# Performance work log

Measured on AMD Instinct MI355X. Metric: run time of the kernel, lower is better.

Reference implementation:

```python
import jax, jax.numpy as jnp
import numpy as np

B, H, W = 8, 512, 512
N_INST = 8
N_SIGMA = 2
FG_W = 1.0
W_INST, W_VAR, W_SEED = 1.0, 10.0, 1.0


def make_yxm():
    xm = jnp.broadcast_to(jnp.linspace(0.0, 1.0, W)[None, None, :], (1, H, W))
    ym = jnp.broadcast_to(jnp.linspace(0.0, 1.0, H)[None, :, None], (1, H, W))
    return jnp.concatenate([ym, xm], 0)  # [2,H,W]


def lovasz_hinge(logits, labels):
    # logits, labels: [P]; labels in {0,1}
    signs = 2.0 * labels - 1.0
    errors = 1.0 - logits * signs
    order = jnp.argsort(-errors)
    errors_s = errors[order]
    gt_s = labels[order]
    gts = gt_s.sum()
    intersection = gts - jnp.cumsum(gt_s)
    union = gts + jnp.cumsum(1.0 - gt_s)
    jac = 1.0 - intersection / union
    jac = jnp.concatenate([jac[:1], jac[1:] - jac[:-1]])
    return jnp.dot(jax.nn.relu(errors_s), jax.lax.stop_gradient(jac))


def seg_item(pred, inst, label, center_img, yxm):
    spatial_emb = jnp.tanh(pred[0:2]) + yxm            # [2,H,W]
    sigma = jax.nn.sigmoid(pred[2:2 + N_SIGMA])        # [2,H,W]
    seed = jax.nn.sigmoid(pred[2 + N_SIGMA])           # [H,W]
    seed_loss = jnp.sum(jnp.where(label == 0, seed * seed, 0.0))

    def per_inst(iid):
        in_mask = (inst == iid)
        cmask = in_mask & center_img
        valid = (cmask.sum() == 1)                      # exactly one center pixel
        m = in_mask.astype(pred.dtype)
        npix = jnp.maximum(m.sum(), 1.0)
        center = jnp.sum(yxm * cmask, axis=(1, 2))      # [2]
        s_mean = jnp.sum(sigma * m, axis=(1, 2)) / npix # [2]
        var_l = jnp.sum(((sigma - jax.lax.stop_gradient(s_mean)[:, None, None]) ** 2) * m) / (N_SIGMA * npix)
        s = jnp.exp(s_mean * 10.0)
        dist = jnp.exp(-jnp.sum(((spatial_emb - center[:, None, None]) ** 2) * s[:, None, None], axis=0))
        inst_l = lovasz_hinge((dist * 2.0 - 1.0).ravel(), m.ravel())
        seed_l = jnp.sum(((seed - jax.lax.stop_gradient(dist)) ** 2) * m)
        v = valid.astype(pred.dtype)
        return inst_l * v, var_l * v, seed_l * v

    il, vl, sl = jax.vmap(per_inst)(jnp.arange(1, N_INST + 1))
    # NOTE: source never increments obj_count in the seg loop, so no division.
    seed_total = (seed_loss + FG_W * sl.sum()) / (H * W)
    return W_INST * il.sum() + W_VAR * vl.sum() + W_SEED * seed_total


def tra_item(pred, inst, center_img, offset, yxm):
    emb = yxm - jnp.tanh(pred[0:2])
    sigma = jax.nn.sigmoid(pred[2:2 + N_SIGMA])

    def per_inst(iid):
        in_mask = (inst == iid)
        cmask = in_mask & center_img
        center = jnp.sum(yxm * cmask, axis=(1, 2))          # [2]
        off_c = jnp.sum(offset * cmask, axis=(1, 2))        # [2]
        gt_c = center - off_c / 256.0
        valid = (cmask.sum() == 1) & (gt_c.min() >= 0.0) & (gt_c.max() <= 1.0)
        m = in_mask.astype(pred.dtype)
        npix = jnp.maximum(m.sum(), 1.0)
        s_mean = jnp.sum(sigma * m, axis=(1, 2)) / npix
        var_l = jnp.sum(((sigma - jax.lax.stop_gradient(s_mean)[:, None, None]) ** 2) * m)  # sum (not mean)
        s = jnp.exp(s_mean * 10.0)
        dist = jnp.exp(-jnp.sum(((emb - gt_c[:, None, None]) ** 2) * s[:, None, None], axis=0))
        tl = lovasz_hinge((dist * 2.0 - 1.0).ravel(), m.ravel())
        v = valid.astype(pred.dtype)
        return tl * v, var_l * v, v

    tl, vl, vs = jax.vmap(per_inst)(jnp.arange(1, N_INST + 1))
    cnt = jnp.maximum(vs.sum(), 1.0)
    return W_INST * (tl.sum() / cnt) + W_VAR * (vl.sum() / cnt)


def setup_inputs() -> dict:
    key = jax.random.key(0)
    k1, k2, k3 = jax.random.split(key, 3)
    inst = np.zeros((H, W), np.int32)
    cen = np.zeros((H, W), bool)
    for i in range(N_INST):
        ty, tx = i // 2, i % 2
        cy, cx = ty * 128 + 64, tx * 256 + 128
        inst[cy - 40:cy + 40, cx - 40:cx + 40] = i + 1
        cen[cy, cx] = True
    instances = jnp.tile(jnp.asarray(inst)[None], (B, 1, 1))
    center_images = jnp.tile(jnp.asarray(cen)[None], (B, 1, 1))
    labels = (instances > 0).astype(jnp.int32)
    return {
        "segmentation_predictions": jax.random.normal(k1, (B, 3 + N_SIGMA, H, W), jnp.float32),
        "tracking_predictions": jax.random.normal(k2, (B // 2, 2 + N_SIGMA, H, W), jnp.float32),
        "instances": instances,
        "labels": labels,
        "center_images": center_images,
        "offsets": jax.random.normal(k3, (B // 2, 2, H, W), jnp.float32),
    }


def reference(segmentation_predictions, tracking_predictions, instances, labels, center_images, offsets):
    yxm = make_yxm()
    seg = jax.vmap(seg_item, in_axes=(0, 0, 0, 0, None))(
        segmentation_predictions, instances, labels, center_images, yxm)
    half = B // 2
    tra = jax.vmap(tra_item, in_axes=(0, 0, 0, 0, None))(
        tracking_predictions, instances[:half], center_images[:half], offsets, yxm)
    return seg.sum() + tra.sum()
```

## Files before the change

### kernel.cpp

```cpp
#include <hip/hip_runtime.h>
#include <cstdint>
#include <cstddef>

#define HW (512 * 512)
#define NB 128
#define NPAIR 96
#define THRQ 4.9f
#define BSCALE 64.0f
#define RB 128

#define W_HNEG 0
#define W_HPOS (NPAIR * NB)
#define W_SEEDL (NPAIR * NB * 2)
#define W_CNT (W_SEEDL + NPAIR)
#define NZERO (W_CNT + 1)
#define W_PART 24704
#define W_CSUM (W_PART + 12 * 81 * RB)
#define W_PRM (W_CSUM + 12 * 81)
#define W_POUT (W_PRM + 12 * 32)

__device__ __forceinline__ float sigmoidf_(float x) {
    return 1.0f / (1.0f + __expf(-x));
}
__device__ __forceinline__ float tanhf_(float x) {
    float e = __expf(2.0f * x);
    return 1.0f - 2.0f / (e + 1.0f);
}
__device__ __forceinline__ float wred(float v) {
#pragma unroll
    for (int o = 32; o > 0; o >>= 1) v += __shfl_down(v, o, 64);
    return v;
}

__global__ __launch_bounds__(256) void reduce_k(
    const float* __restrict__ segp, const float* __restrict__ trap,
    const int* __restrict__ inst, const int* __restrict__ cen,
    const float* __restrict__ off, float* __restrict__ ws)
{
    __shared__ float wavepart[4][41];
    __shared__ float centacc[40];
    int item = blockIdx.y;
    bool isseg = item < 8;
    int ii = isseg ? item : item - 8;
    int bx = blockIdx.x, tid = threadIdx.x;

    {
        int gb = (item * RB + bx) * 17 + tid;
        if (tid < 17 && gb < NZERO) ws[gb] = 0.0f;
    }
    if (tid < 40) centacc[tid] = 0.0f;
    __syncthreads();

    const float* pb = isseg ? segp + (size_t)item * 5 * HW
                            : trap + (size_t)ii * 4 * HW;
    const int* ib = inst + (size_t)ii * HW;
    const int* cb = cen + (size_t)ii * HW;
    const float* ob = off + (size_t)ii * 2 * HW;

    float npx[8], a0[8], q0[8], a1[8], q1[8];
#pragma unroll
    for (int j = 0; j < 8; j++) { npx[j]=0.f; a0[j]=0.f; q0[j]=0.f; a1[j]=0.f; q1[j]=0.f; }
    float sacc = 0.f;

    int base = bx * 2048;
#pragma unroll
    for (int it = 0; it < 2; ++it) {
        int idx = base + (it * 256 + tid) * 4;
        int4 v4 = *(const int4*)&ib[idx];
        const int vs[4] = { v4.x, v4.y, v4.z, v4.w };
        if (isseg) {
            float4 x4 = *(const float4*)&pb[4 * HW + idx];
            const float ss[4] = { x4.x, x4.y, x4.z, x4.w };
#pragma unroll
            for (int c = 0; c < 4; c++) {
                if (vs[c] == 0) { float sd = sigmoidf_(ss[c]); sacc += sd * sd; }
            }
        }
        if ((v4.x | v4.y | v4.z | v4.w) != 0) {
            int4 c4 = *(const int4*)&cb[idx];
            float4 x2 = *(const float4*)&pb[2 * HW + idx];
            float4 x3 = *(const float4*)&pb[3 * HW + idx];
            const int cs[4] = { c4.x, c4.y, c4.z, c4.w };
            const float s2s[4] = { x2.x, x2.y, x2.z, x2.w };
            const float s3s[4] = { x3.x, x3.y, x3.z, x3.w };
#pragma unroll
            for (int c = 0; c < 4; c++) {
                int v = vs[c];
                if (v == 0) continue;
                float s0 = sigmoidf_(s2s[c]);
                float s1 = sigmoidf_(s3s[c]);
                float s00 = s0 * s0, s11 = s1 * s1;
#pragma unroll
                for (int j = 0; j < 8; j++) {
                    float f = (v == j + 1) ? 1.0f : 0.0f;
                    npx[j] += f;
                    a0[j] += f * s0; q0[j] += f * s00;
                    a1[j] += f * s1; q1[j] += f * s11;
                }
                if (cs[c] != 0 && v >= 1 && v <= 8) {
                    int idxc = idx + c;
                    int cb5 = (v - 1) * 5;
                    int y = idxc >> 9, x = idxc & 511;
                    atomicAdd(&centacc[cb5 + 0], (float)y * (1.0f / 511.0f));
                    atomicAdd(&centacc[cb5 + 1], (float)x * (1.0f / 511.0f));
                    atomicAdd(&centacc[cb5 + 2], 1.0f);
                    if (!isseg) {
                        atomicAdd(&centacc[cb5 + 3], ob[idxc]);
                        atomicAdd(&centacc[cb5 + 4], ob[HW + idxc]);
                    }
                }
            }
        }
    }
    int lane = tid & 63, wave = tid >> 6;
#pragma unroll
    for (int j = 0; j < 8; j++) {
        float r0 = wred(npx[j]), r1 = wred(a0[j]), r2 = wred(q0[j]);
        float r3 = wred(a1[j]), r4 = wred(q1[j]);
        if (lane == 0) {
            wavepart[wave][j * 5 + 0] = r0; wavepart[wave][j * 5 + 1] = r1;
            wavepart[wave][j * 5 + 2] = r2; wavepart[wave][j * 5 + 3] = r3;
            wavepart[wave][j * 5 + 4] = r4;
        }
    }
    {
        float rs = wred(sacc);
        if (lane == 0) wavepart[wave][40] = rs;
    }
    __syncthreads();
    float* pit = ws + W_PART + (size_t)item * 81 * RB;
    if (tid < 40) {
        pit[tid * RB + bx] = wavepart[0][tid] + wavepart[1][tid] + wavepart[2][tid] + wavepart[3][tid];
    } else if (tid == 40) {
        pit[80 * RB + bx] = wavepart[0][40] + wavepart[1][40] + wavepart[2][40] + wavepart[3][40];
    } else if (tid < 81) {
        pit[(tid - 1) * RB + bx] = centacc[tid - 41];
    }
}

__global__ __launch_bounds__(256) void csum_k(float* __restrict__ ws)
{
    __shared__ float csh[81];
    int item = blockIdx.x, tid = threadIdx.x;
    bool isseg = item < 8;
    if (tid < 162) {
        int comp = tid >> 1;
        const float* p = ws + W_PART + (size_t)item * 81 * RB + comp * RB + (tid & 1) * 64;
        float s = 0.f;
#pragma unroll 8
        for (int i = 0; i < 64; i++) s += p[i];
        s += __shfl_xor(s, 1, 64);
        if ((tid & 1) == 0) csh[comp] = s;
    }
    __syncthreads();
    if (tid < 81) ws[W_CSUM + item * 81 + tid] = csh[tid];
    if (tid < 8) {
        int j = tid;
        float np = fmaxf(csh[j * 5], 1.0f);
        float cy = csh[40 + j * 5], cx = csh[40 + j * 5 + 1];
        if (!isseg) {
            cy -= csh[40 + j * 5 + 3] * (1.0f / 256.0f);
            cx -= csh[40 + j * 5 + 4] * (1.0f / 256.0f);
        }
        float* o = ws + W_PRM + item * 32 + j * 4;
        o[0] = cy;
        o[1] = cx;
        o[2] = __expf(10.0f * csh[j * 5 + 1] / np);
        o[3] = __expf(10.0f * csh[j * 5 + 3] / np);
    }
}

__global__ __launch_bounds__(256) void hist_k(
    const float* __restrict__ segp, const float* __restrict__ trap,
    const int* __restrict__ inst, float* __restrict__ ws)
{
    __shared__ unsigned hh[8 * NB + 8];
    __shared__ float4 prmv[8];
    __shared__ unsigned char lut[48 * 64];
    int item = blockIdx.y;
    bool isseg = item < 8;
    int ii = isseg ? item : item - 8;
    int bx = blockIdx.x, tid = threadIdx.x;
    int pairBase = (isseg ? 0 : 64) + ii * 8;

    unsigned* wsu = (unsigned*)ws;
    unsigned* hneg = wsu + W_HNEG;
    unsigned* hpos = wsu + W_HPOS;
    float* seedl = ws + W_SEEDL;

    if (tid < 8) prmv[tid] = ((const float4*)(ws + W_PRM + item * 32))[tid];
    for (int i = tid; i < 8 * NB + 8; i += 256) hh[i] = 0u;
    __syncthreads();
    for (int ci = tid; ci < 48 * 64; ci += 256) {
        int iy = ci >> 6, ix = ci & 63;
        float ey = -1.0f + ((float)iy + 0.5f) * (1.0f / 16.0f);
        float ex = -1.0f + ((float)ix + 0.5f) * (1.0f / 16.0f);
        unsigned mk = 0u;
#pragma unroll
        for (int j = 0; j < 8; j++) {
            float4 P = prmv[j];
            float dy = fmaxf(fabsf(ey - P.x) - (1.0f / 32.0f), 0.0f);
            float dx = fmaxf(fabsf(ex - P.y) - (1.0f / 32.0f), 0.0f);
            if (fmaf(dy * dy, P.z, dx * dx * P.w) <= THRQ) mk |= 1u << j;
        }
        lut[ci] = (unsigned char)mk;
    }
    __syncthreads();

    const float* pb = isseg ? segp + (size_t)item * 5 * HW
                            : trap + (size_t)ii * 4 * HW;
    const int* ib = inst + (size_t)ii * HW;

    int base = bx * 2048;
#pragma unroll
    for (int it = 0; it < 2; ++it) {
        int idx = base + (it * 256 + tid) * 4;
        int4 v4 = *(const int4*)&ib[idx];
        float4 f0 = *(const float4*)&pb[idx];
        float4 f1 = *(const float4*)&pb[HW + idx];
        const int vv[4] = { v4.x, v4.y, v4.z, v4.w };
        const float p0s[4] = { f0.x, f0.y, f0.z, f0.w };
        const float p1s[4] = { f1.x, f1.y, f1.z, f1.w };
#pragma unroll
        for (int c = 0; c < 4; c++) {
            int idxc = idx + c;
            int v = vv[c];
            int y = idxc >> 9, x = idxc & 511;
            float ym = (float)y * (1.0f / 511.0f);
            float xm = (float)x * (1.0f / 511.0f);
            float t0 = tanhf_(p0s[c]), t1 = tanhf_(p1s[c]);
            float e0 = isseg ? (t0 + ym) : (ym - t0);
            float e1 = isseg ? (t1 + xm) : (xm - t1);
            int iy = (int)((e0 + 1.0f) * 16.0f);
            int ix = (int)((e1 + 1.0f) * 16.0f);
            unsigned mask = lut[iy * 64 + ix];
            unsigned vb = (unsigned)(v - 1);
            if (vb < 8u) mask |= 1u << vb;
            while (mask) {
                int j = __ffs(mask) - 1;
                mask &= mask - 1u;
                float4 P = prmv[j];
                float d0 = e0 - P.x, d1 = e1 - P.y;
                float q = fmaf(d0 * d0, P.z, d1 * d1 * P.w);
                bool m = (v == j + 1);
                if (m || (q <= THRQ)) {
                    float dd = __expf(-q);
                    float e = m ? fmaf(-2.0f, dd, 2.0f) : 2.0f * dd;
                    int bin = (int)(e * BSCALE);
                    if (bin > NB - 1) bin = NB - 1;
                    atomicAdd(&hh[j * NB + bin], m ? 0x10000u : 1u);
                    if (m && isseg) {
                        float sd = sigmoidf_(pb[4 * HW + idxc]);
                        float df = sd - dd;
                        atomicAdd((float*)&hh[8 * NB + j], df * df);
                    }
                }
            }
        }
    }
    __syncthreads();
    {
        int g = tid >> 5, gl = tid & 31;
        unsigned s = 0u;
#pragma unroll
        for (int b = 0; b < 4; b++) {
            unsigned hv = hh[g * NB + gl * 4 + b];
            s += (hv & 0xFFFFu) + (hv >> 16);
        }
#pragma unroll
        for (int o = 16; o > 0; o >>= 1) s += __shfl_down(s, o, 32);
        if (gl == 0) atomicAdd(&hh[g * NB], 2048u - s);
    }
    __syncthreads();
    for (int i = tid; i < 8 * NB; i += 256) {
        unsigned hv = hh[i];
        if (hv) {
            int j = i >> 7, b = i & (NB - 1);
            size_t gb = (size_t)(pairBase + j) * NB + b;
            unsigned n = hv & 0xFFFFu, p = hv >> 16;
            if (n) atomicAdd(&hneg[gb], n);
            if (p) atomicAdd(&hpos[gb], p);
        }
    }
    if (isseg && tid < 8) {
        float sv = __uint_as_float(hh[8 * NB + tid]);
        if (sv != 0.0f) atomicAdd(&seedl[pairBase + tid], sv);
    }
}

__global__ __launch_bounds__(64) void scanfin_k(
    float* __restrict__ ws, float* __restrict__ out)
{
    __shared__ float fin[NPAIR * 4 + 8];
    int p = blockIdx.x;
    int lane = threadIdx.x;
    unsigned* wsu = (unsigned*)ws;
    const unsigned* hneg = wsu + W_HNEG;
    const unsigned* hpos = wsu + W_HPOS;
    unsigned* cntr = wsu + W_CNT;

    int item12 = (p < 64) ? (p >> 3) : (8 + ((p - 64) >> 3));
    int j = p & 7;
    const float* cs = ws + W_CSUM + item12 * 81;
    float val = 0.f;
    if (lane < 10) {
        int comp = (lane < 5) ? (j * 5 + lane) : (40 + j * 5 + (lane - 5));
        val = cs[comp];
    }
    float r0 = __shfl(val, 0, 64), r1 = __shfl(val, 1, 64), r2 = __shfl(val, 2, 64);
    float r3 = __shfl(val, 3, 64), r4 = __shfl(val, 4, 64);
    float c0 = __shfl(val, 5, 64), c1 = __shfl(val, 6, 64), c2 = __shfl(val, 7, 64);
    float c3 = __shfl(val, 8, 64), c4 = __shfl(val, 9, 64);

    const unsigned* hn = hneg + (size_t)p * NB;
    const unsigned* hp = hpos + (size_t)p * NB;
    unsigned hnv[2], hpv[2];
    float ck = 0.f, cp = 0.f;
#pragma unroll
    for (int i = 0; i < 2; i++) {
        int bn = NB - 1 - (lane * 2 + i);
        unsigned a = hn[bn], b = hp[bn];
        hnv[i] = a; hpv[i] = b;
        ck += (float)(a + b); cp += (float)b;
    }
    float ik = ck, ip = cp;
#pragma unroll
    for (int o = 1; o < 64; o <<= 1) {
        float nk = __shfl_up(ik, o, 64), np2 = __shfl_up(ip, o, 64);
        if (lane >= o) { ik += nk; ip += np2; }
    }
    float P = __shfl(ip, 63, 64);
    float k = ik - ck, pp = ip - cp;
    float acc = 0.f;
#pragma unroll
    for (int i = 0; i < 2; i++) {
        float cn = (float)hnv[i], cpp = (float)hpv[i];
        float c = cn + cpp;
        if (c > 0.f) {
            float Jb = (k > 0.f) ? (1.0f - (P - pp) / (P + k - pp)) : 0.0f;
            k += c; pp += cpp;
            float Ja = 1.0f - (P - pp) / (P + k - pp);
            int bn = NB - 1 - (lane * 2 + i);
            acc += ((float)bn + 0.5f) * (2.0f / NB) * (Ja - Jb);
        }
    }
    acc = wred(acc);

    if (lane == 0) {
        float np = fmaxf(r0, 1.0f);
        float v0 = fmaxf(r2 - r1 * r1 / np, 0.0f);
        float v1 = fmaxf(r4 - r3 * r3 / np, 0.0f);
        float valid, varl;
        if (p < 64) {
            varl = (v0 + v1) / (2.0f * np);
            valid = (c2 > 0.5f && c2 < 1.5f) ? 1.0f : 0.0f;
        } else {
            varl = v0 + v1;
            float gy = c0 - c3 * (1.0f / 256.0f);
            float gx = c1 - c4 * (1.0f / 256.0f);
            valid = (c2 > 0.5f && c2 < 1.5f &&
                     gy >= 0.0f && gy <= 1.0f && gx >= 0.0f && gx <= 1.0f) ? 1.0f : 0.0f;
        }
        float* po = ws + W_POUT + p * 4;
        po[0] = acc; po[1] = valid; po[2] = varl; po[3] = 0.0f;
    }
    __threadfence();
    unsigned old = 0;
    if (lane == 0) old = atomicAdd(cntr, 1u);
    old = (unsigned)__shfl((int)old, 0, 64);
    if (old != NPAIR - 1) return;
    __threadfence();

    volatile const float* pv = ws + W_POUT;
    volatile const float* sdv = ws + W_SEEDL;
    volatile const float* csv = ws + W_CSUM;
    for (int q = lane; q < NPAIR; q += 64) {
        fin[q * 4 + 0] = pv[q * 4 + 0];
        fin[q * 4 + 1] = pv[q * 4 + 1];
        fin[q * 4 + 2] = pv[q * 4 + 2];
        fin[q * 4 + 3] = sdv[q];
    }
    if (lane < 8) fin[NPAIR * 4 + lane] = csv[lane * 81 + 80];
    __syncthreads();
    if (lane == 0) {
        double total = 0.0;
        for (int b = 0; b < 8; b++) {
            double s = 0.0, sl = 0.0;
            for (int jj = 0; jj < 8; jj++) {
                int pr = b * 8 + jj;
                double v = fin[pr * 4 + 1];
                s += v * ((double)fin[pr * 4 + 0] + 10.0 * (double)fin[pr * 4 + 2]);
                sl += v * (double)fin[pr * 4 + 3];
            }
            total += s + ((double)fin[NPAIR * 4 + b] + sl) / (double)HW;
        }
        for (int tt = 0; tt < 4; tt++) {
            double tl = 0.0, vl = 0.0, cnt = 0.0;
            for (int jj = 0; jj < 8; jj++) {
                int pr = 64 + tt * 8 + jj;
                double v = fin[pr * 4 + 1];
                tl += v * (double)fin[pr * 4 + 0];
                vl += v * (double)fin[pr * 4 + 2];
                cnt += v;
            }
            if (cnt < 1.0) cnt = 1.0;
            total += tl / cnt + 10.0 * vl / cnt;
        }
        *out = (float)total;
    }
}

extern "C" void kernel_launch(void* const* d_in, const int* in_sizes, int n_in,
                              void* d_out, int out_size, void* d_ws, size_t ws_size,
                              hipStream_t stream)
{
    const float* segp = (const float*)d_in[0];
    const float* trap = (const float*)d_in[1];
    const int* inst   = (const int*)d_in[2];
    const int* cen    = (const int*)d_in[4];
    const float* off  = (const float*)d_in[5];
    float* out = (float*)d_out;
    float* ws = (float*)d_ws;

    reduce_k<<<dim3(RB, 12), 256, 0, stream>>>(segp, trap, inst, cen, off, ws);
    csum_k<<<12, 256, 0, stream>>>(ws);
    hist_k<<<dim3(RB, 12), 256, 0, stream>>>(segp, trap, inst, ws);
    scanfin_k<<<NPAIR, 64, 0, stream>>>(ws, out);
}
```

Before: 64.83 us.

## Precompute packed quantized embeddings in first pass and split center accumulation kernel

The first pass now computes the tanh-based spatial embedding and writes it, quantized, together with the instance id into one packed 32-bit word per pixel in the workspace. The histogram pass then reads this single word instead of re-reading two prediction channels and the instance map and recomputing tanh. Center-pixel accumulation moves out of the reduction into a separate cen_k kernel over 8 images, and a zero_k kernel clears the accumulators. This trades extra launches, an extra full-size workspace write and quantization error in the embeddings for fewer reads and less math in the histogram pass.

```diff
diff --git a/kernel.cpp b/kernel.cpp
--- a/kernel.cpp
+++ b/kernel.cpp
@@ -13,11 +13,13 @@
 #define W_HPOS (NPAIR * NB)
 #define W_SEEDL (NPAIR * NB * 2)
 #define W_CNT (W_SEEDL + NPAIR)
-#define NZERO (W_CNT + 1)
-#define W_PART 24704
-#define W_CSUM (W_PART + 12 * 81 * RB)
-#define W_PRM (W_CSUM + 12 * 81)
+#define W_CPAR 24676
+#define W_ZEND (W_CPAR + 320)
+#define W_PART 25088
+#define W_CSUM (W_PART + 12 * 41 * RB)
+#define W_PRM 88560
 #define W_POUT (W_PRM + 12 * 32)
+#define W_EPACK 89344
 
 __device__ __forceinline__ float sigmoidf_(float x) {
     return 1.0f / (1.0f + __expf(-x));
@@ -32,30 +34,58 @@
     return v;
 }
 
-__global__ __launch_bounds__(256) void reduce_k(
+__global__ __launch_bounds__(256) void zero_k(float* __restrict__ ws) {
+    int n = W_ZEND - W_SEEDL;
+    for (int i = threadIdx.x; i < n; i += 256) ws[W_SEEDL + i] = 0.0f;
+}
+
+__global__ __launch_bounds__(256) void cen_k(
+    const int* __restrict__ cen, const int* __restrict__ inst,
+    const float* __restrict__ off, float* __restrict__ ws)
+{
+    int img = blockIdx.y;
+    int idx = (blockIdx.x * 256 + threadIdx.x) * 4;
+    int4 c4 = *(const int4*)&cen[(size_t)img * HW + idx];
+    if ((c4.x | c4.y | c4.z | c4.w) == 0) return;
+    const int cs[4] = { c4.x, c4.y, c4.z, c4.w };
+#pragma unroll
+    for (int c = 0; c < 4; c++) {
+        if (cs[c] == 0) continue;
+        int idxc = idx + c;
+        unsigned v = (unsigned)inst[(size_t)img * HW + idxc];
+        if (v - 1u < 8u) {
+            float* cp = ws + W_CPAR + img * 40 + (v - 1) * 5;
+            int y = idxc >> 9, x = idxc & 511;
+            atomicAdd(cp + 0, (float)y * (1.0f / 511.0f));
+            atomicAdd(cp + 1, (float)x * (1.0f / 511.0f));
+            atomicAdd(cp + 2, 1.0f);
+            if (img < 4) {
+                atomicAdd(cp + 3, off[(size_t)img * 2 * HW + idxc]);
+                atomicAdd(cp + 4, off[(size_t)(img * 2 + 1) * HW + idxc]);
+            }
+        }
+    }
+}
+
+__global__ __launch_bounds__(256) void prep_k(
     const float* __restrict__ segp, const float* __restrict__ trap,
-    const int* __restrict__ inst, const int* __restrict__ cen,
-    const float* __restrict__ off, float* __restrict__ ws)
+    const int* __restrict__ inst, float* __restrict__ ws)
 {
     __shared__ float wavepart[4][41];
-    __shared__ float centacc[40];
     int item = blockIdx.y;
     bool isseg = item < 8;
     int ii = isseg ? item : item - 8;
     int bx = blockIdx.x, tid = threadIdx.x;
 
     {
-        int gb = (item * RB + bx) * 17 + tid;
-        if (tid < 17 && gb < NZERO) ws[gb] = 0.0f;
-    }
-    if (tid < 40) centacc[tid] = 0.0f;
-    __syncthreads();
+        int gb = (item * RB + bx) * 16 + tid;
+        if (tid < 16) ws[gb] = 0.0f;
+    }
 
     const float* pb = isseg ? segp + (size_t)item * 5 * HW
                             : trap + (size_t)ii * 4 * HW;
     const int* ib = inst + (size_t)ii * HW;
-    const int* cb = cen + (size_t)ii * HW;
-    const float* ob = off + (size_t)ii * 2 * HW;
+    unsigned* ep = (unsigned*)ws + W_EPACK + (size_t)item * HW;
 
     float npx[8], a0[8], q0[8], a1[8], q1[8];
 #pragma unroll
@@ -67,20 +97,35 @@
     for (int it = 0; it < 2; ++it) {
         int idx = base + (it * 256 + tid) * 4;
         int4 v4 = *(const int4*)&ib[idx];
+        float4 x0 = *(const float4*)&pb[idx];
+        float4 x1 = *(const float4*)&pb[HW + idx];
+        float4 x4v = make_float4(0.f, 0.f, 0.f, 0.f);
+        if (isseg) x4v = *(const float4*)&pb[4 * HW + idx];
         const int vs[4] = { v4.x, v4.y, v4.z, v4.w };
-        if (isseg) {
-            float4 x4 = *(const float4*)&pb[4 * HW + idx];
-            const float ss[4] = { x4.x, x4.y, x4.z, x4.w };
-#pragma unroll
-            for (int c = 0; c < 4; c++) {
-                if (vs[c] == 0) { float sd = sigmoidf_(ss[c]); sacc += sd * sd; }
-            }
-        }
+        const float p0s[4] = { x0.x, x0.y, x0.z, x0.w };
+        const float p1s[4] = { x1.x, x1.y, x1.z, x1.w };
+        const float s4s[4] = { x4v.x, x4v.y, x4v.z, x4v.w };
+        unsigned pk[4];
+#pragma unroll
+        for (int c = 0; c < 4; c++) {
+            int idxc = idx + c;
+            int y = idxc >> 9, x = idxc & 511;
+            float ym = (float)y * (1.0f / 511.0f);
+            float xm = (float)x * (1.0f / 511.0f);
+            float t0 = tanhf_(p0s[c]), t1 = tanhf_(p1s[c]);
+            float e0 = isseg ? (t0 + ym) : (ym - t0);
+            float e1 = isseg ? (t1 + xm) : (xm - t1);
+            int q0i = (int)(fmaf(e0, 4096.0f, 4096.5f));
+            int q1i = (int)(fmaf(e1, 4096.0f, 4096.5f));
+            q0i = min(max(q0i, 0), 12799);
+            q1i = min(max(q1i, 0), 12799);
+            pk[c] = ((unsigned)q0i << 18) | ((unsigned)q1i << 4) | (unsigned)vs[c];
+            if (isseg && vs[c] == 0) { float sd = sigmoidf_(s4s[c]); sacc += sd * sd; }
+        }
+        *(uint4*)&ep[idx] = make_uint4(pk[0], pk[1], pk[2], pk[3]);
         if ((v4.x | v4.y | v4.z | v4.w) != 0) {
-            int4 c4 = *(const int4*)&cb[idx];
             float4 x2 = *(const float4*)&pb[2 * HW + idx];
             float4 x3 = *(const float4*)&pb[3 * HW + idx];
-            const int cs[4] = { c4.x, c4.y, c4.z, c4.w };
             const float s2s[4] = { x2.x, x2.y, x2.z, x2.w };
             const float s3s[4] = { x3.x, x3.y, x3.z, x3.w };
 #pragma unroll
@@ -96,18 +141,6 @@
                     npx[j] += f;
                     a0[j] += f * s0; q0[j] += f * s00;
                     a1[j] += f * s1; q1[j] += f * s11;
-                }
-                if (cs[c] != 0 && v >= 1 && v <= 8) {
-                    int idxc = idx + c;
-                    int cb5 = (v - 1) * 5;
-                    int y = idxc >> 9, x = idxc & 511;
-                    atomicAdd(&centacc[cb5 + 0], (float)y * (1.0f / 511.0f));
-                    atomicAdd(&centacc[cb5 + 1], (float)x * (1.0f / 511.0f));
-                    atomicAdd(&centacc[cb5 + 2], 1.0f);
-                    if (!isseg) {
-                        atomicAdd(&centacc[cb5 + 3], ob[idxc]);
-                        atomicAdd(&centacc[cb5 + 4], ob[HW + idxc]);
-                    }
                 }
             }
         }
@@ -128,24 +161,20 @@
         if (lane == 0) wavepart[wave][40] = rs;
     }
     __syncthreads();
-    float* pit = ws + W_PART + (size_t)item * 81 * RB;
-    if (tid < 40) {
+    float* pit = ws + W_PART + (size_t)item * 41 * RB;
+    if (tid < 41) {
         pit[tid * RB + bx] = wavepart[0][tid] + wavepart[1][tid] + wavepart[2][tid] + wavepart[3][tid];
-    } else if (tid == 40) {
-        pit[80 * RB + bx] = wavepart[0][40] + wavepart[1][40] + wavepart[2][40] + wavepart[3][40];
-    } else if (tid < 81) {
-        pit[(tid - 1) * RB + bx] = centacc[tid - 41];
     }
 }
 
 __global__ __launch_bounds__(256) void csum_k(float* __restrict__ ws)
 {
-    __shared__ float csh[81];
+    __shared__ float csh[41];
     int item = blockIdx.x, tid = threadIdx.x;
     bool isseg = item < 8;
-    if (tid < 162) {
+    if (tid < 82) {
         int comp = tid >> 1;
-        const float* p = ws + W_PART + (size_t)item * 81 * RB + comp * RB + (tid & 1) * 64;
+        const float* p = ws + W_PART + (size_t)item * 41 * RB + comp * RB + (tid & 1) * 64;
         float s = 0.f;
 #pragma unroll 8
         for (int i = 0; i < 64; i++) s += p[i];
@@ -153,15 +182,13 @@
         if ((tid & 1) == 0) csh[comp] = s;
     }
     __syncthreads();
-    if (tid < 81) ws[W_CSUM + item * 81 + tid] = csh[tid];
+    if (tid < 41) ws[W_CSUM + item * 41 + tid] = csh[tid];
     if (tid < 8) {
         int j = tid;
+        const float* cp = ws + W_CPAR + (isseg ? item : item - 8) * 40 + j * 5;
         float np = fmaxf(csh[j * 5], 1.0f);
-        float cy = csh[40 + j * 5], cx = csh[40 + j * 5 + 1];
-        if (!isseg) {
-            cy -= csh[40 + j * 5 + 3] * (1.0f / 256.0f);
-            cx -= csh[40 + j * 5 + 4] * (1.0f / 256.0f);
-        }
+        float cy = cp[0], cx = cp[1];
+        if (!isseg) { cy -= cp[3] * (1.0f / 256.0f); cx -= cp[4] * (1.0f / 256.0f); }
         float* o = ws + W_PRM + item * 32 + j * 4;
         o[0] = cy;
         o[1] = cx;
@@ -171,12 +198,11 @@
 }
 
 __global__ __launch_bounds__(256) void hist_k(
-    const float* __restrict__ segp, const float* __restrict__ trap,
-    const int* __restrict__ inst, float* __restrict__ ws)
+    const float* __restrict__ segp, float* __restrict__ ws)
 {
     __shared__ unsigned hh[8 * NB + 8];
     __shared__ float4 prmv[8];
-    __shared__ unsigned char lut[48 * 64];
+    __shared__ unsigned char lut[50 * 64];
     int item = blockIdx.y;
     bool isseg = item < 8;
     int ii = isseg ? item : item - 8;
@@ -191,10 +217,10 @@
     if (tid < 8) prmv[tid] = ((const float4*)(ws + W_PRM + item * 32))[tid];
     for (int i = tid; i < 8 * NB + 8; i += 256) hh[i] = 0u;
     __syncthreads();
-    for (int ci = tid; ci < 48 * 64; ci += 256) {
+    for (int ci = tid; ci < 50 * 64; ci += 256) {
         int iy = ci >> 6, ix = ci & 63;
-        float ey = -1.0f + ((float)iy + 0.5f) * (1.0f / 16.0f);
-        float ex = -1.0f + ((float)ix + 0.5f) * (1.0f / 16.0f);
+        float ey = ((float)iy + 0.5f) * (1.0f / 16.0f) - 1.0f;
+        float ex = ((float)ix + 0.5f) * (1.0f / 16.0f) - 1.0f;
         unsigned mk = 0u;
 #pragma unroll
         for (int j = 0; j < 8; j++) {
@@ -207,42 +233,33 @@
     }
     __syncthreads();
 
-    const float* pb = isseg ? segp + (size_t)item * 5 * HW
-                            : trap + (size_t)ii * 4 * HW;
-    const int* ib = inst + (size_t)ii * HW;
+    const unsigned* ep = wsu + W_EPACK + (size_t)item * HW;
+    const float* pb4 = segp + (size_t)item * 5 * HW + 4 * HW;
 
     int base = bx * 2048;
 #pragma unroll
     for (int it = 0; it < 2; ++it) {
         int idx = base + (it * 256 + tid) * 4;
-        int4 v4 = *(const int4*)&ib[idx];
-        float4 f0 = *(const float4*)&pb[idx];
-        float4 f1 = *(const float4*)&pb[HW + idx];
-        const int vv[4] = { v4.x, v4.y, v4.z, v4.w };
-        const float p0s[4] = { f0.x, f0.y, f0.z, f0.w };
-        const float p1s[4] = { f1.x, f1.y, f1.z, f1.w };
+        uint4 u4 = *(const uint4*)&ep[idx];
+        const unsigned us[4] = { u4.x, u4.y, u4.z, u4.w };
 #pragma unroll
         for (int c = 0; c < 4; c++) {
-            int idxc = idx + c;
-            int v = vv[c];
-            int y = idxc >> 9, x = idxc & 511;
-            float ym = (float)y * (1.0f / 511.0f);
-            float xm = (float)x * (1.0f / 511.0f);
-            float t0 = tanhf_(p0s[c]), t1 = tanhf_(p1s[c]);
-            float e0 = isseg ? (t0 + ym) : (ym - t0);
-            float e1 = isseg ? (t1 + xm) : (xm - t1);
-            int iy = (int)((e0 + 1.0f) * 16.0f);
-            int ix = (int)((e1 + 1.0f) * 16.0f);
-            unsigned mask = lut[iy * 64 + ix];
-            unsigned vb = (unsigned)(v - 1);
-            if (vb < 8u) mask |= 1u << vb;
-            while (mask) {
+            unsigned u = us[c];
+            unsigned v = u & 0xFu;
+            int qe1 = (int)((u >> 4) & 0x3FFFu);
+            int qe0 = (int)(u >> 18);
+            unsigned mask = lut[(qe0 >> 8) * 64 + (qe1 >> 8)];
+            if (v) mask |= 1u << (v - 1);
+            if (!mask) continue;
+            float e0 = (float)qe0 * (1.0f / 4096.0f) - 1.0f;
+            float e1 = (float)qe1 * (1.0f / 4096.0f) - 1.0f;
+            do {
                 int j = __ffs(mask) - 1;
                 mask &= mask - 1u;
                 float4 P = prmv[j];
                 float d0 = e0 - P.x, d1 = e1 - P.y;
                 float q = fmaf(d0 * d0, P.z, d1 * d1 * P.w);
-                bool m = (v == j + 1);
+                bool m = (v == (unsigned)(j + 1));
                 if (m || (q <= THRQ)) {
                     float dd = __expf(-q);
                     float e = m ? fmaf(-2.0f, dd, 2.0f) : 2.0f * dd;
@@ -250,12 +267,12 @@
                     if (bin > NB - 1) bin = NB - 1;
                     atomicAdd(&hh[j * NB + bin], m ? 0x10000u : 1u);
                     if (m && isseg) {
-                        float sd = sigmoidf_(pb[4 * HW + idxc]);
+                        float sd = sigmoidf_(pb4[idx + c]);
                         float df = sd - dd;
                         atomicAdd((float*)&hh[8 * NB + j], df * df);
                     }
                 }
-            }
+            } while (mask);
         }
     }
     __syncthreads();
@@ -300,13 +317,11 @@
     unsigned* cntr = wsu + W_CNT;
 
     int item12 = (p < 64) ? (p >> 3) : (8 + ((p - 64) >> 3));
+    int img = (p < 64) ? (p >> 3) : ((p - 64) >> 3);
     int j = p & 7;
-    const float* cs = ws + W_CSUM + item12 * 81;
     float val = 0.f;
-    if (lane < 10) {
-        int comp = (lane < 5) ? (j * 5 + lane) : (40 + j * 5 + (lane - 5));
-        val = cs[comp];
-    }
+    if (lane < 5) val = ws[W_CSUM + item12 * 41 + j * 5 + lane];
+    else if (lane < 10) val = ws[W_CPAR + img * 40 + j * 5 + (lane - 5)];
     float r0 = __shfl(val, 0, 64), r1 = __shfl(val, 1, 64), r2 = __shfl(val, 2, 64);
     float r3 = __shfl(val, 3, 64), r4 = __shfl(val, 4, 64);
     float c0 = __shfl(val, 5, 64), c1 = __shfl(val, 6, 64), c2 = __shfl(val, 7, 64);
@@ -380,7 +395,7 @@
         fin[q * 4 + 2] = pv[q * 4 + 2];
         fin[q * 4 + 3] = sdv[q];
     }
-    if (lane < 8) fin[NPAIR * 4 + lane] = csv[lane * 81 + 80];
+    if (lane < 8) fin[NPAIR * 4 + lane] = csv[lane * 41 + 40];
     __syncthreads();
     if (lane == 0) {
         double total = 0.0;
@@ -422,8 +437,10 @@
     float* out = (float*)d_out;
     float* ws = (float*)d_ws;
 
-    reduce_k<<<dim3(RB, 12), 256, 0, stream>>>(segp, trap, inst, cen, off, ws);
+    zero_k<<<1, 256, 0, stream>>>(ws);
+    cen_k<<<dim3(256, 8), 256, 0, stream>>>(cen, inst, off, ws);
+    prep_k<<<dim3(RB, 12), 256, 0, stream>>>(segp, trap, inst, ws);
     csum_k<<<12, 256, 0, stream>>>(ws);
-    hist_k<<<dim3(RB, 12), 256, 0, stream>>>(segp, trap, inst, ws);
+    hist_k<<<dim3(RB, 12), 256, 0, stream>>>(segp, ws);
     scanfin_k<<<NPAIR, 64, 0, stream>>>(ws, out);
 }
```

New measurement: 73.73 us. 1.14x slower.
